# Kernel tuning notes

Measured on AMD Instinct MI355X. Metric: run time of the kernel, lower is better.

Reference implementation:

```python
import jax, jax.numpy as jnp
import numpy as np
from jax import lax

N, C, H, W = 1, 3, 480, 640
K_LCN = 9
K_ASW = 12
SIGMA_OMEGA = 2.0
LCN_WEIGHT = 0.5
OCC_WEIGHT = 0.1
LN2 = 0.6931


def _box_filter(x, k):
    # depthwise kxk mean filter, zero ('same') padding — matches F.conv2d(groups=3)
    w = jnp.ones((C, 1, k, k), x.dtype) / (k * k)
    return lax.conv_general_dilated(
        x, w, (1, 1), [(k // 2, k // 2)] * 2,
        dimension_numbers=('NCHW', 'OIHW', 'NCHW'), feature_group_count=C)


def _lcn(img, k=K_LCN):
    mean = _box_filter(img, k)
    msq = _box_filter(img ** 2, k)
    std = jnp.sqrt(jax.nn.relu(msq - mean ** 2)) * (k * k) / (k * k - 1)
    return (img - mean) / (std + 1e-5), std


def _sample_x(img, x):
    # grid_sample with identity y and x-only shift reduces to horizontal linear
    # interpolation with zero padding (align_corners=False pixel-center math).
    Wd = img.shape[-1]
    x0 = jnp.floor(x)
    w1 = x - x0
    x0i = x0.astype(jnp.int32)
    def gather(xi):
        valid = ((xi >= 0) & (xi < Wd)).astype(img.dtype)
        return jnp.take_along_axis(img, jnp.clip(xi, 0, Wd - 1), axis=-1) * valid
    return gather(x0i) * (1 - w1) + gather(x0i + 1) * w1


def _resample(img, disp_other, disp_guide, sign):
    # sample img and disp_other at x = j + sign*disp_guide (left view: sign=-1)
    xs = jnp.arange(W, dtype=img.dtype) + sign * disp_guide  # [N,1,H,W]
    recon_img = _sample_x(img, jnp.broadcast_to(xs, img.shape))
    recon_disp = _sample_x(disp_other, xs)
    return recon_img, recon_disp


def _asw(guide, cost, k=K_ASW, sigma=SIGMA_OMEGA):
    # adaptive support-weight (bilateral) aggregation over a kxk window,
    # zero-padded, window offsets -k//2 .. k//2-1 (even k, as in the original)
    pad = k // 2
    gp = jnp.pad(guide, ((0, 0), (0, 0), (pad, pad), (pad, pad)))
    cp = jnp.pad(cost, ((0, 0), (0, 0), (pad, pad), (pad, pad)))
    shape = guide.shape
    def body(carry, idx):
        wg, ca = carry
        i = idx // k
        j = idx % k
        gs = lax.dynamic_slice(gp, (0, 0, i, j), shape)
        cs = lax.dynamic_slice(cp, (0, 0, i, j), shape)
        t = jnp.exp(-jnp.abs(guide - gs) / sigma)
        return (wg + t, ca + t * cs), None
    init = (jnp.zeros(shape, guide.dtype), jnp.zeros(shape, guide.dtype))
    (wg, ca), _ = lax.scan(body, init, jnp.arange(k * k, dtype=jnp.int32))
    return ca / wg


def _ce_ones_target(p):
    # CrossEntropyLoss(mean) with logits [1-p, p] and target class 1 everywhere
    logits = jnp.concatenate([1.0 - p, p], axis=1)  # [N,2,H,W]
    ls = jax.nn.log_softmax(logits, axis=1)
    return -jnp.mean(ls[:, 1])


def _forward(left_img, right_img, dispmap_left, dispmap_right, weight):
    recon_img_right, recon_disp_right = _resample(right_img, dispmap_right, dispmap_left, -1.0)
    recon_img_left, recon_disp_left = _resample(left_img, dispmap_left, dispmap_right, 1.0)

    losses_left_photo = jnp.abs(left_img - recon_img_right)
    losses_right_photo = jnp.abs(right_img - recon_img_left)

    rir_lcn, _ = _lcn(recon_img_right)
    ril_lcn, _ = _lcn(recon_img_left)
    l_lcn, l_std = _lcn(left_img)
    r_lcn, r_std = _lcn(right_img)
    losses_left_lcn = _asw(left_img, jnp.abs((l_lcn - rir_lcn) * l_std))
    # NOTE: original uses left_img as the ASW guide for the right loss too
    losses_right_lcn = _asw(left_img, jnp.abs((r_lcn - ril_lcn) * r_std))

    losses_left = (1 - LCN_WEIGHT) * losses_left_photo + LCN_WEIGHT * losses_left_lcn
    losses_right = (1 - LCN_WEIGHT) * losses_right_photo + LCN_WEIGHT * losses_right_lcn

    p_left = jnp.exp(-LN2 * jnp.abs(dispmap_left - recon_disp_right))   # [N,1,H,W]
    p_right = jnp.exp(-LN2 * jnp.abs(dispmap_right - recon_disp_left))

    loss_invalid = _ce_ones_target(p_left) + _ce_ones_target(p_right)

    mask_left = (p_left > 0.5).astype(losses_left.dtype)    # broadcasts over C=3
    mask_right = (p_right > 0.5).astype(losses_right.dtype)
    loss_valid = (jnp.sum(losses_left * mask_left) / (C * jnp.sum(mask_left) + 1e-6)
                  + jnp.sum(losses_right * mask_right) / (C * jnp.sum(mask_right) + 1e-6))

    return weight * ((1 - OCC_WEIGHT) * loss_valid + OCC_WEIGHT * loss_invalid)


def setup_inputs() -> dict:
    key = jax.random.key(0)
    k1, k2, k3, k4, k5 = jax.random.split(key, 5)
    return {
        'left_img': jax.random.uniform(k1, (N, C, H, W), dtype=jnp.float32),
        'right_img': jax.random.uniform(k2, (N, C, H, W), dtype=jnp.float32),
        'dispmap_left': jax.random.uniform(k3, (N, 1, H, W), dtype=jnp.float32) * 32.0,
        'dispmap_right': jax.random.uniform(k4, (N, 1, H, W), dtype=jnp.float32) * 32.0,
        'dispmap_gt': jax.random.uniform(k5, (N, 1, H, W), dtype=jnp.float32) * 32.0,
        'brk': 0,
        'weight': jnp.asarray(1.0, dtype=jnp.float32),
    }


def reference(left_img, right_img, dispmap_left, dispmap_right, dispmap_gt, brk, weight):
    # dispmap_gt and brk are accepted but unused by the original forward math
    return _forward(left_img, right_img, dispmap_left, dispmap_right, weight)
```

## Files before the change

### kernel.cpp

```cpp
#include <hip/hip_runtime.h>
#include <math.h>

#define HH 480
#define WW 640
#define HW (HH*WW)

#define NB1 1200
#define NB3 3600

__device__ __forceinline__ unsigned bf16rne(float f) {
    unsigned u = __float_as_uint(f);
    return (u + 0x7fffu + ((u >> 16) & 1u)) >> 16;
}


__device__ __forceinline__ float sample1(const float* __restrict__ row, float x) {
    float x0 = floorf(x);
    float w1 = x - x0;
    int xi = (int)x0;
    float v0 = (xi >= 0 && xi < WW) ? row[xi] : 0.f;
    float v1 = (xi + 1 >= 0 && xi + 1 < WW) ? row[xi + 1] : 0.f;
    return v0 * (1.f - w1) + v1 * w1;
}

__global__ __launch_bounds__(256) void k_resample(
    const float* __restrict__ left, const float* __restrict__ right,
    const float* __restrict__ dispL, const float* __restrict__ dispR,
    float* __restrict__ rir, float* __restrict__ ril,
    unsigned char* __restrict__ maskb, float* __restrict__ part1)
{
    __shared__ float red[4][6];
    int tid = threadIdx.x;
    int idx = blockIdx.x * blockDim.x + tid;
    int h = idx / WW;
    int w = idx - h * WW;
    float dL = dispL[idx];
    float dR = dispR[idx];
    float xl = (float)w - dL;
    float xr = (float)w + dR;
    float photoL = 0.f, photoR = 0.f;
    #pragma unroll
    for (int c = 0; c < 3; ++c) {
        float rv = sample1(right + c*HW + h*WW, xl);
        float lv = sample1(left  + c*HW + h*WW, xr);
        rir[c*HW + idx] = rv;
        ril[c*HW + idx] = lv;
        photoL += fabsf(left [c*HW + idx] - rv);
        photoR += fabsf(right[c*HW + idx] - lv);
    }
    float rdr = sample1(dispR + h*WW, xl);
    float rdl = sample1(dispL + h*WW, xr);
    float pl = __expf(-0.6931f * fabsf(dL - rdr));
    float pr = __expf(-0.6931f * fabsf(dR - rdl));
    float mL = (pl > 0.5f) ? 1.f : 0.f;
    float mR = (pr > 0.5f) ? 1.f : 0.f;
    maskb[idx] = (unsigned char)((mL > 0.f ? 1u : 0u) | (mR > 0.f ? 2u : 0u));

    float vals[6];
    vals[0] = 0.5f * photoL * mL;
    vals[1] = mL;
    vals[2] = 0.5f * photoR * mR;
    vals[3] = mR;
    vals[4] = log1pf(__expf(1.f - 2.f * pl));
    vals[5] = log1pf(__expf(1.f - 2.f * pr));

    int lane = tid & 63, wave = tid >> 6;
    #pragma unroll
    for (int k = 0; k < 6; ++k) {
        float v = vals[k];
        #pragma unroll
        for (int off = 32; off > 0; off >>= 1) v += __shfl_down(v, off);
        if (lane == 0) red[wave][k] = v;
    }
    __syncthreads();
    if (tid < 6)
        part1[blockIdx.x * 8 + tid] =
            red[0][tid] + red[1][tid] + red[2][tid] + red[3][tid];
}


__global__ __launch_bounds__(256) void k_lcnpack(
    const float* __restrict__ left, const float* __restrict__ right,
    const float* __restrict__ rir, const float* __restrict__ ril,
    unsigned* __restrict__ epem,
    unsigned short* __restrict__ cl16, unsigned short* __restrict__ cr16)
{
    __shared__ float raw[2][16][40];
    __shared__ float2 hsp[2][16][32];
    int tx = threadIdx.x, ty = threadIdx.y;
    int tid = ty * 32 + tx;
    int gx0 = blockIdx.x * 32, gy0 = blockIdx.y * 8;
    int side = blockIdx.z & 1, ch = blockIdx.z >> 1;
    const float* __restrict__ A = (side ? right : left) + ch*HW;
    const float* __restrict__ B = (side ? ril   : rir) + ch*HW;

    for (int e = tid; e < 2*16*40; e += 256) {
        int a   = e >> 9;
        int rem = e & 511;
        int r   = rem / 40;
        int x   = rem - r * 40;
        int gy = gy0 + r - 4, gx = gx0 + x - 4;
        float v = 0.f;
        if ((unsigned)gy < (unsigned)HH && (unsigned)gx < (unsigned)WW)
            v = (a ? B : A)[gy*WW + gx];
        ((float*)raw)[e] = v;
    }
    __syncthreads();

    {
        int f   = tid;
        int a   = f >> 7;
        int rem = f & 127;
        int r   = rem >> 3;
        int x0  = (rem & 7) * 4;
        const float* row = &raw[a][r][x0];
        float4 p0 = *(const float4*)(row);
        float4 p1 = *(const float4*)(row + 4);
        float4 p2 = *(const float4*)(row + 8);
        float v[12] = {p0.x, p0.y, p0.z, p0.w, p1.x, p1.y, p1.z, p1.w,
                       p2.x, p2.y, p2.z, p2.w};
        float sq[12];
        #pragma unroll
        for (int i = 0; i < 12; ++i) sq[i] = v[i] * v[i];
        float s0 = v[0]+v[1]+v[2]+v[3]+v[4]+v[5]+v[6]+v[7]+v[8];
        float q0 = sq[0]+sq[1]+sq[2]+sq[3]+sq[4]+sq[5]+sq[6]+sq[7]+sq[8];
        float s1 = s0 - v[0] + v[9];
        float q1 = q0 - sq[0] + sq[9];
        float s2 = s1 - v[1] + v[10];
        float q2 = q1 - sq[1] + sq[10];
        float s3 = s2 - v[2] + v[11];
        float q3 = q2 - sq[2] + sq[11];
        float4* out = (float4*)&hsp[a][r][x0];
        out[0] = make_float4(s0, q0, s1, q1);
        out[1] = make_float4(s2, q2, s3, q3);
    }
    __syncthreads();

    int idx = ch*HW + (gy0 + ty) * WW + gx0 + tx;
    float SA = 0.f, SA2 = 0.f, SB = 0.f, SB2 = 0.f;
    #pragma unroll
    for (int dy = 0; dy < 9; ++dy) {
        float2 ha = hsp[0][ty + dy][tx];
        float2 hb = hsp[1][ty + dy][tx];
        SA  += ha.x;
        SA2 += ha.y;
        SB  += hb.x;
        SB2 += hb.y;
    }
    float meanA = SA * (1.f/81.f);
    float stdA  = sqrtf(fmaxf(SA2 * (1.f/81.f) - meanA * meanA, 0.f)) * (81.f/80.f);
    float lcnA  = (raw[0][ty + 4][tx + 4] - meanA) / (stdA + 1e-5f);
    float meanB = SB * (1.f/81.f);
    float stdB  = sqrtf(fmaxf(SB2 * (1.f/81.f) - meanB * meanB, 0.f)) * (81.f/80.f);
    float lcnB  = (raw[1][ty + 4][tx + 4] - meanB) / (stdB + 1e-5f);
    float cost  = fabsf((lcnA - lcnB) * stdA);
    if (side == 0) {
        float g = raw[0][ty + 4][tx + 4];
        epem[idx] = bf16rne(__expf(0.5f * g)) | (bf16rne(__expf(-0.5f * g)) << 16);
        cl16[idx] = (unsigned short)bf16rne(cost);
    } else {
        cr16[idx] = (unsigned short)bf16rne(cost);
    }
}


#define T3H 19
#define T3W 43

__global__ __launch_bounds__(64) void k_asw_reduce(
    const unsigned* __restrict__ epem,
    const unsigned short* __restrict__ cl16, const unsigned short* __restrict__ cr16,
    const unsigned char* __restrict__ maskb,
    float* __restrict__ part3)
{
    __shared__ float4 tile[T3H][T3W];
    int tx = threadIdx.x, ty = threadIdx.y;
    int tid = tx + 32 * ty;
    int c = blockIdx.z;
    int gx0 = blockIdx.x * 32, gy0 = blockIdx.y * 8;

    for (int e = tid; e < T3H * T3W; e += 64) {
        int r   = e / T3W;
        int x   = e - r * T3W;
        int gy = gy0 + r - 6, gx = gx0 + x - 6;
        float4 v = make_float4(1.f, 1.f, 0.f, 0.f);
        if ((unsigned)gy < (unsigned)HH && (unsigned)gx < (unsigned)WW) {
            int o = c*HW + gy*WW + gx;
            unsigned pe = epem[o];
            v.x = __uint_as_float(pe << 16);
            v.y = __uint_as_float(pe & 0xffff0000u);
            v.z = __uint_as_float((unsigned)cl16[o] << 16);
            v.w = __uint_as_float((unsigned)cr16[o] << 16);
        }
        tile[r][x] = v;
    }
    __syncthreads();

    int ty4 = 4 * ty;
    float epc[4], emc[4];
    #pragma unroll
    for (int i = 0; i < 4; ++i) {
        float4 cv = tile[ty4 + i + 6][tx + 6];
        epc[i] = cv.x;
        emc[i] = cv.y;
    }

    float wg[4] = {0.f,0.f,0.f,0.f}, aL[4] = {0.f,0.f,0.f,0.f}, aR[4] = {0.f,0.f,0.f,0.f};

    auto taprow = [&](int kap, int i0, int i1) {
        const float4* row = &tile[ty4 + kap][tx];
        #pragma unroll
        for (int dx = 0; dx < 12; ++dx) {
            float4 v = row[dx];
            #pragma unroll
            for (int i = 0; i < 4; ++i) {
                if (i >= i0 && i <= i1) {
                    float t = fminf(emc[i] * v.x, epc[i] * v.y);
                    wg[i] += t;
                    aL[i] = fmaf(t, v.z, aL[i]);
                    aR[i] = fmaf(t, v.w, aR[i]);
                }
            }
        }
    };

    taprow(0, 0, 0);
    taprow(1, 0, 1);
    taprow(2, 0, 2);
    for (int kap = 3; kap <= 11; ++kap)
        taprow(kap, 0, 3);
    taprow(12, 1, 3);
    taprow(13, 2, 3);
    taprow(14, 3, 3);

    float v0 = 0.f, v2 = 0.f;
    #pragma unroll
    for (int i = 0; i < 4; ++i) {
        int idx = (gy0 + ty4 + i) * WW + gx0 + tx;
        unsigned m = maskb[idx];
        float aswL = aL[i] / wg[i];
        float aswR = aR[i] / wg[i];
        if (m & 1u) v0 += 0.5f * aswL;
        if (m & 2u) v2 += 0.5f * aswR;
    }

    #pragma unroll
    for (int off = 32; off > 0; off >>= 1) {
        v0 += __shfl_down(v0, off);
        v2 += __shfl_down(v2, off);
    }
    if (tid == 0) {
        int bid = (blockIdx.z * gridDim.y + blockIdx.y) * gridDim.x + blockIdx.x;
        part3[bid * 8 + 0] = v0;
        part3[bid * 8 + 1] = v2;
    }
}


__global__ __launch_bounds__(256) void k_final(
    const float* __restrict__ part1, const float* __restrict__ part3,
    const float* __restrict__ weight, float* __restrict__ out)
{
    __shared__ float red[4][6];
    int tid = threadIdx.x;
    float v[6] = {0.f, 0.f, 0.f, 0.f, 0.f, 0.f};
    for (int b = tid; b < NB1; b += 256) {
        #pragma unroll
        for (int k = 0; k < 6; ++k) v[k] += part1[b * 8 + k];
    }
    for (int b = tid; b < NB3; b += 256) {
        v[0] += part3[b * 8 + 0];
        v[2] += part3[b * 8 + 1];
    }
    int lane = tid & 63, wave = tid >> 6;
    #pragma unroll
    for (int k = 0; k < 6; ++k) {
        float s = v[k];
        #pragma unroll
        for (int off = 32; off > 0; off >>= 1) s += __shfl_down(s, off);
        if (lane == 0) red[wave][k] = s;
    }
    __syncthreads();
    if (tid == 0) {
        float a[6];
        #pragma unroll
        for (int k = 0; k < 6; ++k)
            a[k] = red[0][k] + red[1][k] + red[2][k] + red[3][k];
        float loss_valid = a[0] / (3.f * a[1] + 1e-6f) + a[2] / (3.f * a[3] + 1e-6f);
        float loss_invalid = (a[4] + a[5]) * (1.f / (float)HW);
        out[0] = weight[0] * (0.9f * loss_valid + 0.1f * loss_invalid);
    }
}


extern "C" void kernel_launch(void* const* d_in, const int* in_sizes, int n_in,
                              void* d_out, int out_size, void* d_ws, size_t ws_size,
                              hipStream_t stream)
{
    const float* left  = (const float*)d_in[0];
    const float* right = (const float*)d_in[1];
    const float* dispL = (const float*)d_in[2];
    const float* dispR = (const float*)d_in[3];
    const float* weight = (const float*)d_in[6];

    float* ws    = (float*)d_ws;
    float* rir   = ws;
    float* ril   = rir + 3*HW;
    unsigned* epem = (unsigned*)(ws + 6*HW);
    unsigned short* cl16 = (unsigned short*)(ws + 9*HW);
    unsigned short* cr16 = (unsigned short*)(ws + 9*HW) + 3*HW;
    unsigned char* maskb = (unsigned char*)(ws + 12*HW);
    float* part1 = ws + 12*HW + HW/4;
    float* part3 = part1 + NB1*8;

    k_resample<<<NB1, 256, 0, stream>>>(left, right, dispL, dispR, rir, ril, maskb, part1);

    dim3 blk2(32, 8);
    dim3 grd2(WW / 32, HH / 8, 6);
    k_lcnpack<<<grd2, blk2, 0, stream>>>(left, right, rir, ril, epem, cl16, cr16);

    dim3 blk3(32, 2);
    dim3 grd3(WW / 32, HH / 8, 3);
    k_asw_reduce<<<grd3, blk3, 0, stream>>>(epem, cl16, cr16, maskb, part3);

    k_final<<<1, 256, 0, stream>>>(part1, part3, weight, (float*)d_out);
}
```

Measured before the change: 75.77 us.

## Split ASW tap rows across two wave groups and pack shared tile as bf16

The ASW aggregation block doubles to 128 threads. Each half computes a subset of the 15 tap rows, and the partial weight and cost sums are combined through shared memory before the masked reduction. The shared tile now stores packed bf16 pairs (uint2) instead of float4, which halves LDS footprint and read bandwidth but adds unpacking ALU work per tap. The lcnpack load-index decode is also fixed (e/640 instead of e>>9), which corrects the raw tile addressing.

New measurement: 103.2 us. +36.2%, slower.

```diff
diff --git a/kernel.cpp b/kernel.cpp
--- a/kernel.cpp
+++ b/kernel.cpp
@@ -95,8 +95,8 @@
     const float* __restrict__ B = (side ? ril   : rir) + ch*HW;
 
     for (int e = tid; e < 2*16*40; e += 256) {
-        int a   = e >> 9;
-        int rem = e & 511;
+        int a   = e / 640;
+        int rem = e - a * 640;
         int r   = rem / 40;
         int x   = rem - r * 40;
         int gy = gy0 + r - 4, gx = gx0 + x - 4;
@@ -167,30 +167,28 @@
 #define T3H 19
 #define T3W 43
 
-__global__ __launch_bounds__(64) void k_asw_reduce(
+__global__ __launch_bounds__(128) void k_asw_reduce(
     const unsigned* __restrict__ epem,
     const unsigned short* __restrict__ cl16, const unsigned short* __restrict__ cr16,
     const unsigned char* __restrict__ maskb,
     float* __restrict__ part3)
 {
-    __shared__ float4 tile[T3H][T3W];
-    int tx = threadIdx.x, ty = threadIdx.y;
-    int tid = tx + 32 * ty;
+    __shared__ uint2 tile[T3H][T3W];
+    __shared__ float part[2][4][3][32];
+    int tx = threadIdx.x, ty = threadIdx.y, wz = threadIdx.z;
+    int tid = tx + 32 * ty + 64 * wz;
     int c = blockIdx.z;
     int gx0 = blockIdx.x * 32, gy0 = blockIdx.y * 8;
 
-    for (int e = tid; e < T3H * T3W; e += 64) {
+    for (int e = tid; e < T3H * T3W; e += 128) {
         int r   = e / T3W;
         int x   = e - r * T3W;
         int gy = gy0 + r - 6, gx = gx0 + x - 6;
-        float4 v = make_float4(1.f, 1.f, 0.f, 0.f);
+        uint2 v = make_uint2(0x3f803f80u, 0u);
         if ((unsigned)gy < (unsigned)HH && (unsigned)gx < (unsigned)WW) {
             int o = c*HW + gy*WW + gx;
-            unsigned pe = epem[o];
-            v.x = __uint_as_float(pe << 16);
-            v.y = __uint_as_float(pe & 0xffff0000u);
-            v.z = __uint_as_float((unsigned)cl16[o] << 16);
-            v.w = __uint_as_float((unsigned)cr16[o] << 16);
+            v.x = epem[o];
+            v.y = (unsigned)cl16[o] | ((unsigned)cr16[o] << 16);
         }
         tile[r][x] = v;
     }
@@ -200,59 +198,82 @@
     float epc[4], emc[4];
     #pragma unroll
     for (int i = 0; i < 4; ++i) {
-        float4 cv = tile[ty4 + i + 6][tx + 6];
-        epc[i] = cv.x;
-        emc[i] = cv.y;
+        unsigned vc = tile[ty4 + i + 6][tx + 6].x;
+        epc[i] = __uint_as_float(vc << 16);
+        emc[i] = __uint_as_float(vc & 0xffff0000u);
     }
 
     float wg[4] = {0.f,0.f,0.f,0.f}, aL[4] = {0.f,0.f,0.f,0.f}, aR[4] = {0.f,0.f,0.f,0.f};
 
     auto taprow = [&](int kap, int i0, int i1) {
-        const float4* row = &tile[ty4 + kap][tx];
+        const uint2* row = &tile[ty4 + kap][tx];
         #pragma unroll
         for (int dx = 0; dx < 12; ++dx) {
-            float4 v = row[dx];
+            uint2 v = row[dx];
+            float ep  = __uint_as_float(v.x << 16);
+            float em  = __uint_as_float(v.x & 0xffff0000u);
+            float clv = __uint_as_float(v.y << 16);
+            float crv = __uint_as_float(v.y & 0xffff0000u);
             #pragma unroll
             for (int i = 0; i < 4; ++i) {
                 if (i >= i0 && i <= i1) {
-                    float t = fminf(emc[i] * v.x, epc[i] * v.y);
+                    float t = fminf(emc[i] * ep, epc[i] * em);
                     wg[i] += t;
-                    aL[i] = fmaf(t, v.z, aL[i]);
-                    aR[i] = fmaf(t, v.w, aR[i]);
+                    aL[i] = fmaf(t, clv, aL[i]);
+                    aR[i] = fmaf(t, crv, aR[i]);
                 }
             }
         }
     };
 
-    taprow(0, 0, 0);
-    taprow(1, 0, 1);
-    taprow(2, 0, 2);
-    for (int kap = 3; kap <= 11; ++kap)
-        taprow(kap, 0, 3);
-    taprow(12, 1, 3);
-    taprow(13, 2, 3);
-    taprow(14, 3, 3);
-
-    float v0 = 0.f, v2 = 0.f;
-    #pragma unroll
-    for (int i = 0; i < 4; ++i) {
-        int idx = (gy0 + ty4 + i) * WW + gx0 + tx;
-        unsigned m = maskb[idx];
-        float aswL = aL[i] / wg[i];
-        float aswR = aR[i] / wg[i];
-        if (m & 1u) v0 += 0.5f * aswL;
-        if (m & 2u) v2 += 0.5f * aswR;
-    }
-
-    #pragma unroll
-    for (int off = 32; off > 0; off >>= 1) {
-        v0 += __shfl_down(v0, off);
-        v2 += __shfl_down(v2, off);
-    }
-    if (tid == 0) {
-        int bid = (blockIdx.z * gridDim.y + blockIdx.y) * gridDim.x + blockIdx.x;
-        part3[bid * 8 + 0] = v0;
-        part3[bid * 8 + 1] = v2;
+    if (wz == 0) {
+        taprow(0, 0, 0);
+        taprow(1, 0, 1);
+        taprow(2, 0, 2);
+        taprow(3, 0, 3);
+        taprow(4, 0, 3);
+        taprow(5, 0, 3);
+        taprow(6, 0, 3);
+        taprow(7, 0, 3);
+    } else {
+        taprow(8, 0, 3);
+        taprow(9, 0, 3);
+        taprow(10, 0, 3);
+        taprow(11, 0, 3);
+        taprow(12, 1, 3);
+        taprow(13, 2, 3);
+        taprow(14, 3, 3);
+        #pragma unroll
+        for (int i = 0; i < 4; ++i) {
+            part[ty][i][0][tx] = wg[i];
+            part[ty][i][1][tx] = aL[i];
+            part[ty][i][2][tx] = aR[i];
+        }
+    }
+    __syncthreads();
+
+    if (wz == 0) {
+        float v0 = 0.f, v2 = 0.f;
+        #pragma unroll
+        for (int i = 0; i < 4; ++i) {
+            float w  = wg[i] + part[ty][i][0][tx];
+            float l  = aL[i] + part[ty][i][1][tx];
+            float r  = aR[i] + part[ty][i][2][tx];
+            int idx = (gy0 + ty4 + i) * WW + gx0 + tx;
+            unsigned m = maskb[idx];
+            if (m & 1u) v0 += 0.5f * (l / w);
+            if (m & 2u) v2 += 0.5f * (r / w);
+        }
+        #pragma unroll
+        for (int off = 32; off > 0; off >>= 1) {
+            v0 += __shfl_down(v0, off);
+            v2 += __shfl_down(v2, off);
+        }
+        if (tid == 0) {
+            int bid = (blockIdx.z * gridDim.y + blockIdx.y) * gridDim.x + blockIdx.x;
+            part3[bid * 8 + 0] = v0;
+            part3[bid * 8 + 1] = v2;
+        }
     }
 }
 
@@ -319,7 +340,7 @@
     dim3 grd2(WW / 32, HH / 8, 6);
     k_lcnpack<<<grd2, blk2, 0, stream>>>(left, right, rir, ril, epem, cl16, cr16);
 
-    dim3 blk3(32, 2);
+    dim3 blk3(32, 2, 2);
     dim3 grd3(WW / 32, HH / 8, 3);
     k_asw_reduce<<<grd3, blk3, 0, stream>>>(epem, cl16, cr16, maskb, part3);
 
```
